# Performance work log

Measured on AMD Instinct MI355X. Metric: run time of the kernel, lower is better.

## Reference

```python
import jax, jax.numpy as jnp
import numpy as np

NEG_INF = -1e30
D_MODEL = 128


def setup_inputs() -> dict:
    key = jax.random.key(0)
    k1, k2, k3 = jax.random.split(key, 3)
    B, D, Lc, Lq = 64, D_MODEL, 1024, 256
    C = jax.random.normal(k1, (B, D, Lc), dtype=jnp.float32)
    Q = jax.random.normal(k2, (B, D, Lq), dtype=jnp.float32)
    cmask = jnp.ones((B, Lc), dtype=jnp.float32)
    qmask = jnp.ones((B, Lq), dtype=jnp.float32)
    lim = (1.0 / D) ** 0.5
    w = jax.random.uniform(k3, (3 * D,), dtype=jnp.float32, minval=-lim, maxval=lim)
    return {"C": C, "Q": Q, "cmask": cmask, "qmask": qmask, "w": w}


def reference(C, Q, cmask, qmask, w):
    # C: (B, D, Lc), Q: (B, D, Lq), w: (3D,)
    D = C.shape[1]
    Ct = jnp.swapaxes(C, 1, 2)  # (B, Lc, D)
    Qt = jnp.swapaxes(Q, 1, 2)  # (B, Lq, D)
    w1, w2, w3 = w[:D], w[D:2 * D], w[2 * D:]
    # Decomposed trilinear similarity: equivalent to cat([Ct,Qt,Ct*Qt]) @ w
    S = (jnp.einsum('bld,d->bl', Ct, w1)[:, :, None]
         + jnp.einsum('bmd,d->bm', Qt, w2)[:, None, :]
         + jnp.einsum('bld,bmd->blm', Ct * w3, Qt))  # (B, Lc, Lq)
    qm = qmask[:, None, :]  # (B, 1, Lq)
    cm = cmask[:, :, None]  # (B, Lc, 1)
    S1 = jax.nn.softmax(S + (1.0 - qm) * NEG_INF, axis=2)
    S2 = jax.nn.softmax(S + (1.0 - cm) * NEG_INF, axis=1)
    A = jnp.einsum('blm,bmd->bld', S1, Qt)  # (B, Lc, D)
    S12 = jnp.einsum('blm,bnm->bln', S1, S2)  # (B, Lc, Lc)
    Bv = jnp.einsum('bln,bnd->bld', S12, Ct)  # (B, Lc, D)
    out = jnp.concatenate([Ct, A, Ct * A, Ct * Bv], axis=2)  # (B, Lc, 4D)
    # dropout is identity in eval mode
    return jnp.swapaxes(out, 1, 2)  # (B, 4D, Lc)
```

## Files before the change

kernel.cpp:

```cpp
#include <hip/hip_runtime.h>

#define NB  64
#define ND  128
#define NLC 1024
#define NLQ 256
#define FNEG (-1e30f)

typedef __bf16 bf16x8 __attribute__((ext_vector_type(8)));
typedef float f32x4 __attribute__((ext_vector_type(4)));

__device__ __forceinline__ ushort f2bf(float x) {
  unsigned u = __float_as_uint(x);
  return (ushort)((u + 0x7fffu + ((u >> 16) & 1u)) >> 16);
}
__device__ __forceinline__ float bf2f(ushort u) {
  return __uint_as_float((unsigned)u << 16);
}
__device__ __forceinline__ bf16x8 ldfrag(const ushort* p) {
  return *reinterpret_cast<const bf16x8*>(p);
}
__device__ __forceinline__ uint4 pack8(float a0, float a1, float a2, float a3,
                                       float a4, float a5, float a6, float a7) {
  uint4 pk;
  pk.x = (unsigned)f2bf(a0) | ((unsigned)f2bf(a1) << 16);
  pk.y = (unsigned)f2bf(a2) | ((unsigned)f2bf(a3) << 16);
  pk.z = (unsigned)f2bf(a4) | ((unsigned)f2bf(a5) << 16);
  pk.w = (unsigned)f2bf(a6) | ((unsigned)f2bf(a7) << 16);
  return pk;
}

__global__ __launch_bounds__(256) void convert_kernel(
    const float* __restrict__ C, const float* __restrict__ Q,
    const float* __restrict__ w,
    ushort* __restrict__ Ctw3, ushort* __restrict__ Qt16,
    ushort* __restrict__ Cn16, ushort* __restrict__ Qn16,
    float* __restrict__ c1part, float* __restrict__ q2part) {
  __shared__ float tile[64][65];
  __shared__ float cred[64][4];
  int b = blockIdx.y;
  int tid = blockIdx.x;
  int t = threadIdx.x, c = t & 63, r0 = t >> 6;
  if (tid < 32) {
    int d0 = (tid >> 4) * 64, l0 = (tid & 15) * 64;
    const float* src = C + (size_t)b * ND * NLC;
    float part = 0.f;
#pragma unroll
    for (int p = 0; p < 16; ++p) {
      int r = r0 + p * 4;
      float v = src[(size_t)(d0 + r) * NLC + l0 + c];
      tile[c][r] = v * w[2 * ND + d0 + r];
      part += v * w[d0 + r];
    }
    cred[c][r0] = part;
    __syncthreads();
    ushort* dst = Ctw3 + (size_t)b * NLC * ND;
#pragma unroll
    for (int p = 0; p < 16; ++p) {
      int r = r0 + p * 4;
      dst[(size_t)(l0 + r) * ND + d0 + c] = f2bf(tile[r][c]);
    }
    if (t < 64)
      c1part[(size_t)(tid >> 4) * NB * NLC + b * NLC + l0 + t] =
          cred[t][0] + cred[t][1] + cred[t][2] + cred[t][3];
  } else if (tid < 40) {
    int q = tid - 32;
    int d0 = (q >> 2) * 64, m0 = (q & 3) * 64;
    const float* src = Q + (size_t)b * ND * NLQ;
    float part = 0.f;
#pragma unroll
    for (int p = 0; p < 16; ++p) {
      int r = r0 + p * 4;
      float v = src[(size_t)(d0 + r) * NLQ + m0 + c];
      tile[c][r] = v;
      part += v * w[ND + d0 + r];
    }
    cred[c][r0] = part;
    __syncthreads();
    ushort* dst = Qt16 + (size_t)b * NLQ * ND;
#pragma unroll
    for (int p = 0; p < 16; ++p) {
      int r = r0 + p * 4;
      dst[(size_t)(m0 + r) * ND + d0 + c] = f2bf(tile[r][c]);
    }
    if (t < 64)
      q2part[(size_t)(q >> 2) * NB * NLQ + b * NLQ + m0 + t] =
          cred[t][0] + cred[t][1] + cred[t][2] + cred[t][3];
  } else if (tid < 56) {
    size_t ofs = (size_t)(tid - 40) * 8192;
    const float* src = C + (size_t)b * ND * NLC + ofs;
    ushort* dst = Cn16 + (size_t)b * ND * NLC + ofs;
#pragma unroll
    for (int it = 0; it < 4; ++it) {
      int e = (it * 256 + t) * 8;
      float4 v0 = *(const float4*)(src + e), v1 = *(const float4*)(src + e + 4);
      *(uint4*)(dst + e) = pack8(v0.x, v0.y, v0.z, v0.w, v1.x, v1.y, v1.z, v1.w);
    }
  } else {
    size_t ofs = (size_t)(tid - 56) * 16384;
    const float* src = Q + (size_t)b * ND * NLQ + ofs;
    ushort* dst = Qn16 + (size_t)b * ND * NLQ + ofs;
#pragma unroll
    for (int it = 0; it < 8; ++it) {
      int e = (it * 256 + t) * 8;
      float4 v0 = *(const float4*)(src + e), v1 = *(const float4*)(src + e + 4);
      *(uint4*)(dst + e) = pack8(v0.x, v0.y, v0.z, v0.w, v1.x, v1.y, v1.z, v1.w);
    }
  }
}

__global__ __launch_bounds__(512) void score_stats(
    const ushort* __restrict__ Ctw3, const ushort* __restrict__ Qt16,
    const ushort* __restrict__ Cn16,
    const float* __restrict__ c1part, const float* __restrict__ q2part,
    const float* __restrict__ cmask, const float* __restrict__ qmask,
    ushort* __restrict__ e1g, float* __restrict__ rscale_g,
    float* __restrict__ psum_part, float* __restrict__ chunkmax_g,
    float* __restrict__ Tpart) {
  __shared__ union {
    struct { __align__(16) ushort As[128 * 32]; __align__(16) ushort Bs[256 * 32]; } s;
    __align__(16) ushort bounce[128 * 264];
    struct { __align__(16) ushort bounce2[256 * 136]; __align__(16) ushort As_c[4 * 128 * 32]; } t2;
  } u;
  __shared__ float rowred[128][4];
  __shared__ float rowsum[128][4];
  __shared__ float colred[256][2];
  __shared__ float rmaxs[128];
  __shared__ float rcs[128];
  __shared__ float cnegs[128];
  __shared__ float qnegs[256];
  __shared__ float c1s[128];
  __shared__ float q2s[256];
  __shared__ float chunkmax_s;

  int b = blockIdx.y, chunk = blockIdx.x, l0 = chunk * 128;
  int t = threadIdx.x, lane = t & 63, wid = t >> 6;
  int wy = wid >> 2, wx = wid & 3, ln = lane & 15, qd = lane >> 4;

  if (t < 128) {
    int idx = b * NLC + l0 + t;
    c1s[t] = c1part[idx] + c1part[NB * NLC + idx];
    cnegs[t] = (1.f - cmask[idx]) * FNEG;
  } else if (t < 384) {
    int m = t - 128;
    int idx = b * NLQ + m;
    q2s[m] = q2part[idx] + q2part[NB * NLQ + idx];
    qnegs[m] = (1.f - qmask[idx]) * FNEG;
  }

  const ushort* Ab = Ctw3 + (size_t)b * NLC * ND;
  const ushort* Bb = Qt16 + (size_t)b * NLQ * ND;
  f32x4 acc[4][4];
#pragma unroll
  for (int i = 0; i < 4; ++i)
#pragma unroll
    for (int j = 0; j < 4; ++j) acc[i][j] = (f32x4){0.f, 0.f, 0.f, 0.f};

  for (int kk = 0; kk < ND; kk += 32) {
#pragma unroll
    for (int p = 0; p < 3; ++p) {
      int e4 = p * 512 + t;
      if (e4 < 512) {
        int r = e4 >> 2, cc = (e4 & 3) * 8;
        *(int4*)(u.s.As + r * 32 + cc) = *(const int4*)(Ab + (size_t)(l0 + r) * ND + kk + cc);
      } else {
        int e = e4 - 512;
        int r = e >> 2, cc = (e & 3) * 8;
        *(int4*)(u.s.Bs + r * 32 + cc) = *(const int4*)(Bb + (size_t)r * ND + kk + cc);
      }
    }
    __syncthreads();
    bf16x8 af[4], bfr[4];
#pragma unroll
    for (int i = 0; i < 4; ++i) {
      af[i]  = ldfrag(u.s.As + (wy * 64 + i * 16 + ln) * 32 + qd * 8);
      bfr[i] = ldfrag(u.s.Bs + (wx * 64 + i * 16 + ln) * 32 + qd * 8);
    }
#pragma unroll
    for (int i = 0; i < 4; ++i)
#pragma unroll
      for (int j = 0; j < 4; ++j)
        acc[i][j] = __builtin_amdgcn_mfma_f32_16x16x32_bf16(af[i], bfr[j], acc[i][j], 0, 0, 0);
    __syncthreads();
  }

  float qnj[4], q2j[4];
#pragma unroll
  for (int j = 0; j < 4; ++j) {
    int m = wx * 64 + j * 16 + ln;
    qnj[j] = qnegs[m];
    q2j[j] = q2s[m];
  }
#pragma unroll
  for (int i = 0; i < 4; ++i)
#pragma unroll
    for (int r = 0; r < 4; ++r) {
      int ll = wy * 64 + i * 16 + qd * 4 + r;
      float cv = c1s[ll];
#pragma unroll
      for (int j = 0; j < 4; ++j) acc[i][j][r] += cv + q2j[j];
    }

#pragma unroll
  for (int i = 0; i < 4; ++i)
#pragma unroll
    for (int r = 0; r < 4; ++r) {
      float v = -INFINITY;
#pragma unroll
      for (int j = 0; j < 4; ++j) v = fmaxf(v, acc[i][j][r] + qnj[j]);
      v = fmaxf(v, __shfl_xor(v, 1));
      v = fmaxf(v, __shfl_xor(v, 2));
      v = fmaxf(v, __shfl_xor(v, 4));
      v = fmaxf(v, __shfl_xor(v, 8));
      if (ln == 0) rowred[wy * 64 + i * 16 + qd * 4 + r][wx] = v;
    }
  __syncthreads();
  if (t < 128) {
    float v = fmaxf(fmaxf(rowred[t][0], rowred[t][1]), fmaxf(rowred[t][2], rowred[t][3]));
    rmaxs[t] = v;
    rcs[t] = v + cnegs[t];
  }
  __syncthreads();
  if (t < 64) {
    float v = fmaxf(rcs[t], rcs[t + 64]);
    v = fmaxf(v, __shfl_xor(v, 1));
    v = fmaxf(v, __shfl_xor(v, 2));
    v = fmaxf(v, __shfl_xor(v, 4));
    v = fmaxf(v, __shfl_xor(v, 8));
    v = fmaxf(v, __shfl_xor(v, 16));
    v = fmaxf(v, __shfl_xor(v, 32));
    if (t == 0) chunkmax_s = v;
  }
  __syncthreads();
  if (t < 128) rcs[t] = __expf(rcs[t] - chunkmax_s);
  __syncthreads();

  float cs[4] = {0.f, 0.f, 0.f, 0.f};
#pragma unroll
  for (int i = 0; i < 4; ++i)
#pragma unroll
    for (int r = 0; r < 4; ++r) {
      int ll = wy * 64 + i * 16 + qd * 4 + r;
      float rmx = rmaxs[ll], rf = rcs[ll];
      float rs = 0.f;
#pragma unroll
      for (int j = 0; j < 4; ++j) {
        float e = __expf(acc[i][j][r] + qnj[j] - rmx);
        acc[i][j][r] = e;
        rs += e;
        cs[j] += e * rf;
      }
      rs += __shfl_xor(rs, 1);
      rs += __shfl_xor(rs, 2);
      rs += __shfl_xor(rs, 4);
      rs += __shfl_xor(rs, 8);
      if (ln == 0) rowsum[ll][wx] = rs;
    }
#pragma unroll
  for (int j = 0; j < 4; ++j) {
    float v = cs[j];
    v += __shfl_xor(v, 16);
    v += __shfl_xor(v, 32);
    if (qd == 0) colred[wx * 64 + j * 16 + ln][wy] = v;
  }
  __syncthreads();
  if (t < 128)
    rscale_g[b * NLC + l0 + t] =
        1.f / (rowsum[t][0] + rowsum[t][1] + rowsum[t][2] + rowsum[t][3]);
  if (t >= 256 && t < 512) {
    int m = t - 256;
    psum_part[(b * 8 + chunk) * NLQ + m] = colred[m][0] + colred[m][1];
  }
  if (t == 0) chunkmax_g[b * 8 + chunk] = chunkmax_s;

#pragma unroll
  for (int i = 0; i < 4; ++i)
#pragma unroll
    for (int r = 0; r < 4; ++r) {
      int ll = wy * 64 + i * 16 + qd * 4 + r;
#pragma unroll
      for (int j = 0; j < 4; ++j)
        u.bounce[ll * 264 + wx * 64 + j * 16 + ln] = f2bf(acc[i][j][r]);
    }
  __syncthreads();
  ushort* Eb = e1g + (size_t)b * NLC * NLQ;
#pragma unroll
  for (int p = 0; p < 8; ++p) {
    int idx4 = p * 512 + t;
    int r = idx4 >> 5, c = (idx4 & 31) * 8;
    *(int4*)(Eb + (size_t)(l0 + r) * NLQ + c) = *(const int4*)(u.bounce + r * 264 + c);
  }
  __syncthreads();

#pragma unroll
  for (int i = 0; i < 4; ++i)
#pragma unroll
    for (int r = 0; r < 4; ++r) {
      int ll = wy * 64 + i * 16 + qd * 4 + r;
      float rf = rcs[ll];
#pragma unroll
      for (int j = 0; j < 4; ++j)
        u.t2.bounce2[(wx * 64 + j * 16 + ln) * 136 + ll] = f2bf(acc[i][j][r] * rf);
    }
  {
    const ushort* Cb = Cn16 + (size_t)b * ND * NLC;
#pragma unroll
    for (int p = 0; p < 4; ++p) {
      int e4 = p * 512 + t;
      int slab = e4 >> 9, rr = (e4 >> 2) & 127, cc = (e4 & 3) * 8;
      *(int4*)(u.t2.As_c + slab * (128 * 32) + rr * 32 + cc) =
          *(const int4*)(Cb + (size_t)rr * NLC + l0 + slab * 32 + cc);
    }
  }
  __syncthreads();
  f32x4 acc2[4][4];
#pragma unroll
  for (int i = 0; i < 4; ++i)
#pragma unroll
    for (int j = 0; j < 4; ++j) acc2[i][j] = (f32x4){0.f, 0.f, 0.f, 0.f};
#pragma unroll
  for (int kk = 0; kk < 4; ++kk) {
    bf16x8 af2[4], bf2[4];
#pragma unroll
    for (int i = 0; i < 4; ++i)
      af2[i] = ldfrag(u.t2.As_c + kk * (128 * 32) + (wy * 64 + i * 16 + ln) * 32 + qd * 8);
#pragma unroll
    for (int j = 0; j < 4; ++j)
      bf2[j] = ldfrag(u.t2.bounce2 + (wx * 64 + j * 16 + ln) * 136 + kk * 32 + qd * 8);
#pragma unroll
    for (int i = 0; i < 4; ++i)
#pragma unroll
      for (int j = 0; j < 4; ++j)
        acc2[i][j] = __builtin_amdgcn_mfma_f32_16x16x32_bf16(af2[i], bf2[j], acc2[i][j], 0, 0, 0);
  }
  float* Tb = Tpart + (size_t)(b * 8 + chunk) * ND * NLQ;
#pragma unroll
  for (int i = 0; i < 4; ++i)
#pragma unroll
    for (int r = 0; r < 4; ++r) {
      int d = wy * 64 + i * 16 + qd * 4 + r;
#pragma unroll
      for (int j = 0; j < 4; ++j) {
        int m = wx * 64 + j * 16 + ln;
        Tb[(size_t)d * NLQ + m] = acc2[i][j][r];
      }
    }
}

__global__ __launch_bounds__(256) void stat_combine(
    const float* __restrict__ psum_part, const float* __restrict__ chunkmax_g,
    float* __restrict__ cinv) {
  __shared__ float cm[8];
  int b = blockIdx.x, t = threadIdx.x;
  if (t < 8) cm[t] = chunkmax_g[b * 8 + t];
  __syncthreads();
  float K = cm[0];
#pragma unroll
  for (int c = 1; c < 8; ++c) K = fmaxf(K, cm[c]);
  float s = 0.f;
#pragma unroll
  for (int c = 0; c < 8; ++c)
    s += psum_part[(b * 8 + c) * NLQ + t] * __expf(cm[c] - K);
  cinv[b * NLQ + t] = 1.f / s;
}

__global__ __launch_bounds__(256) void tcombine(
    const float* __restrict__ Tpart, const float* __restrict__ cinv,
    const float* __restrict__ chunkmax_g, ushort* __restrict__ Tt) {
  int gid = blockIdx.x * 256 + threadIdx.x;
  int e = gid * 4;
  int b = e >> 15;
  int r = e & 32767;
  int m = r & 255;
  const float* cmb = chunkmax_g + b * 8;
  float K = cmb[0];
#pragma unroll
  for (int c = 1; c < 8; ++c) K = fmaxf(K, cmb[c]);
  float4 s = {0.f, 0.f, 0.f, 0.f};
#pragma unroll
  for (int c = 0; c < 8; ++c) {
    float fac = __expf(cmb[c] - K);
    float4 v = *(const float4*)(Tpart + ((size_t)(b * 8 + c)) * ND * NLQ + r);
    s.x += fac * v.x; s.y += fac * v.y; s.z += fac * v.z; s.w += fac * v.w;
  }
  float4 ci = *(const float4*)(cinv + b * NLQ + m);
  ushort4 o;
  o.x = f2bf(s.x * ci.x); o.y = f2bf(s.y * ci.y);
  o.z = f2bf(s.z * ci.z); o.w = f2bf(s.w * ci.w);
  *(ushort4*)(Tt + (size_t)b * ND * NLQ + r) = o;
}

__global__ __launch_bounds__(512) void outk(
    const float* __restrict__ C, const ushort* __restrict__ Qn16,
    const ushort* __restrict__ Tt, const ushort* __restrict__ e1g,
    const float* __restrict__ rscale, float* __restrict__ out) {
  __shared__ __align__(16) ushort As1[128 * 32];
  __shared__ __align__(16) ushort As2[128 * 32];
  __shared__ __align__(16) ushort Bs[256 * 32];
  int b = blockIdx.y;
  int l0 = blockIdx.x * 256;
  const ushort* Qb = Qn16 + (size_t)b * ND * NLQ;
  const ushort* Tb = Tt + (size_t)b * ND * NLQ;
  const ushort* Eb = e1g + (size_t)b * NLC * NLQ;
  int t = threadIdx.x, lane = t & 63, wid = t >> 6, wy = wid >> 2, wx = wid & 3;
  int ln = lane & 15, qd = lane >> 4;
  f32x4 acc1[4][4], acc2[4][4];
#pragma unroll
  for (int i = 0; i < 4; ++i)
#pragma unroll
    for (int j = 0; j < 4; ++j) {
      acc1[i][j] = (f32x4){0.f, 0.f, 0.f, 0.f};
      acc2[i][j] = (f32x4){0.f, 0.f, 0.f, 0.f};
    }

  for (int m0 = 0; m0 < NLQ; m0 += 32) {
    {
      int r = t >> 2, cc = (t & 3) * 8;
      *(int4*)(As1 + r * 32 + cc) = *(const int4*)(Qb + (size_t)r * NLQ + m0 + cc);
      *(int4*)(As2 + r * 32 + cc) = *(const int4*)(Tb + (size_t)r * NLQ + m0 + cc);
    }
#pragma unroll
    for (int p = 0; p < 2; ++p) {
      int e4 = p * 512 + t;
      int r = e4 >> 2, cc = (e4 & 3) * 8;
      *(int4*)(Bs + r * 32 + cc) = *(const int4*)(Eb + (size_t)(l0 + r) * NLQ + m0 + cc);
    }
    __syncthreads();
    bf16x8 a1[4], a2[4], bfr[4];
#pragma unroll
    for (int i = 0; i < 4; ++i) {
      a1[i] = ldfrag(As1 + (wy * 64 + i * 16 + ln) * 32 + qd * 8);
      a2[i] = ldfrag(As2 + (wy * 64 + i * 16 + ln) * 32 + qd * 8);
      bfr[i] = ldfrag(Bs + (wx * 64 + i * 16 + ln) * 32 + qd * 8);
    }
#pragma unroll
    for (int i = 0; i < 4; ++i)
#pragma unroll
      for (int j = 0; j < 4; ++j) {
        acc1[i][j] = __builtin_amdgcn_mfma_f32_16x16x32_bf16(a1[i], bfr[j], acc1[i][j], 0, 0, 0);
        acc2[i][j] = __builtin_amdgcn_mfma_f32_16x16x32_bf16(a2[i], bfr[j], acc2[i][j], 0, 0, 0);
      }
    __syncthreads();
  }

  const float* Cb = C + (size_t)b * ND * NLC;
  float* outb = out + (size_t)b * 4 * ND * NLC;
#pragma unroll
  for (int j = 0; j < 4; ++j) {
    int l = l0 + wx * 64 + j * 16 + ln;
    float rs = rscale[b * NLC + l];
#pragma unroll
    for (int i = 0; i < 4; ++i)
#pragma unroll
      for (int r = 0; r < 4; ++r) {
        int d = wy * 64 + i * 16 + qd * 4 + r;
        float a = acc1[i][j][r] * rs;
        float bv = acc2[i][j][r] * rs;
        float c = Cb[(size_t)d * NLC + l];
        outb[(size_t)d * NLC + l] = c;
        outb[(size_t)(128 + d) * NLC + l] = a;
        outb[(size_t)(256 + d) * NLC + l] = c * a;
        outb[(size_t)(384 + d) * NLC + l] = c * bv;
      }
  }
}

extern "C" void kernel_launch(void* const* d_in, const int* in_sizes, int n_in,
                              void* d_out, int out_size, void* d_ws, size_t ws_size,
                              hipStream_t stream) {
  const float* C     = (const float*)d_in[0];
  const float* Q     = (const float*)d_in[1];
  const float* cmask = (const float*)d_in[2];
  const float* qmask = (const float*)d_in[3];
  const float* w     = (const float*)d_in[4];
  float* out = (float*)d_out;

  char* p = (char*)d_ws;
  auto alloc = [&](size_t bytes) { char* r = p; p += (bytes + 255) & ~(size_t)255; return r; };
  ushort* e1g    = (ushort*)alloc((size_t)NB * NLC * NLQ * 2);
  ushort* Ctw3   = (ushort*)alloc((size_t)NB * NLC * ND * 2);
  ushort* Qt16   = (ushort*)alloc((size_t)NB * NLQ * ND * 2);
  ushort* Cn16   = (ushort*)alloc((size_t)NB * ND * NLC * 2);
  ushort* Qn16   = (ushort*)alloc((size_t)NB * ND * NLQ * 2);
  float*  Tpart  = (float*)alloc((size_t)NB * 8 * ND * NLQ * 4);
  ushort* Tt     = (ushort*)alloc((size_t)NB * ND * NLQ * 2);
  float*  c1part = (float*)alloc((size_t)2 * NB * NLC * 4);
  float*  q2part = (float*)alloc((size_t)2 * NB * NLQ * 4);
  float*  rscale = (float*)alloc((size_t)NB * NLC * 4);
  float*  cinv   = (float*)alloc((size_t)NB * NLQ * 4);
  float*  psum   = (float*)alloc((size_t)NB * 8 * NLQ * 4);
  float*  chmax  = (float*)alloc((size_t)NB * 8 * 4);

  convert_kernel<<<dim3(58, NB), 256, 0, stream>>>(C, Q, w, Ctw3, Qt16, Cn16, Qn16,
                                                   c1part, q2part);
  score_stats<<<dim3(NLC / 128, NB), 512, 0, stream>>>(
      Ctw3, Qt16, Cn16, c1part, q2part, cmask, qmask, e1g, rscale, psum, chmax, Tpart);
  stat_combine<<<NB, 256, 0, stream>>>(psum, chmax, cinv);
  tcombine<<<(NB * ND * NLQ / 4) / 256, 256, 0, stream>>>(Tpart, cinv, chmax, Tt);
  outk<<<dim3(NLC / 256, NB), 512, 0, stream>>>(C, Qn16, Tt, e1g, rscale, out);
}
```

Before: 307.0 us.

## Register-prefetch next K tile, shrink shared memory, retile outk for occupancy

Both GEMM kernels now prefetch the next K-slice into registers while computing on the current shared-memory tile, which overlaps global loads with MFMA work. score_stats folds its reduction scratch into the shared-memory union and reads C fragments straight from global memory instead of staging them, freeing LDS so more blocks can reside per CU (launch bounds now request 4). outk is retiled to 256 threads and 128-column blocks with a min-blocks hint of 2, doubling the grid. The trade-offs are higher register pressure from the prefetch buffers, uncoalesced global fragment loads in the second GEMM, and an extra barrier.

```diff
diff --git a/kernel.cpp b/kernel.cpp
--- a/kernel.cpp
+++ b/kernel.cpp
@@ -108,7 +108,7 @@
   }
 }
 
-__global__ __launch_bounds__(512) void score_stats(
+__global__ __launch_bounds__(512, 4) void score_stats(
     const ushort* __restrict__ Ctw3, const ushort* __restrict__ Qt16,
     const ushort* __restrict__ Cn16,
     const float* __restrict__ c1part, const float* __restrict__ q2part,
@@ -118,12 +118,10 @@
     float* __restrict__ Tpart) {
   __shared__ union {
     struct { __align__(16) ushort As[128 * 32]; __align__(16) ushort Bs[256 * 32]; } s;
+    struct { float rowred[128][4]; float rowsum[128][4]; float colred[256][2]; } red;
     __align__(16) ushort bounce[128 * 264];
-    struct { __align__(16) ushort bounce2[256 * 136]; __align__(16) ushort As_c[4 * 128 * 32]; } t2;
+    __align__(16) ushort bounce2[256 * 136];
   } u;
-  __shared__ float rowred[128][4];
-  __shared__ float rowsum[128][4];
-  __shared__ float colred[256][2];
   __shared__ float rmaxs[128];
   __shared__ float rcs[128];
   __shared__ float cnegs[128];
@@ -155,20 +153,50 @@
 #pragma unroll
     for (int j = 0; j < 4; ++j) acc[i][j] = (f32x4){0.f, 0.f, 0.f, 0.f};
 
-  for (int kk = 0; kk < ND; kk += 32) {
+  int4 va[3];
+  {
 #pragma unroll
     for (int p = 0; p < 3; ++p) {
       int e4 = p * 512 + t;
       if (e4 < 512) {
         int r = e4 >> 2, cc = (e4 & 3) * 8;
-        *(int4*)(u.s.As + r * 32 + cc) = *(const int4*)(Ab + (size_t)(l0 + r) * ND + kk + cc);
+        va[p] = *(const int4*)(Ab + (size_t)(l0 + r) * ND + 0 + cc);
       } else {
         int e = e4 - 512;
         int r = e >> 2, cc = (e & 3) * 8;
-        *(int4*)(u.s.Bs + r * 32 + cc) = *(const int4*)(Bb + (size_t)r * ND + kk + cc);
-      }
-    }
+        va[p] = *(const int4*)(Bb + (size_t)r * ND + 0 + cc);
+      }
+    }
+  }
+  for (int kk = 0; kk < ND; kk += 32) {
     __syncthreads();
+#pragma unroll
+    for (int p = 0; p < 3; ++p) {
+      int e4 = p * 512 + t;
+      if (e4 < 512) {
+        int r = e4 >> 2, cc = (e4 & 3) * 8;
+        *(int4*)(u.s.As + r * 32 + cc) = va[p];
+      } else {
+        int e = e4 - 512;
+        int r = e >> 2, cc = (e & 3) * 8;
+        *(int4*)(u.s.Bs + r * 32 + cc) = va[p];
+      }
+    }
+    __syncthreads();
+    if (kk + 32 < ND) {
+#pragma unroll
+      for (int p = 0; p < 3; ++p) {
+        int e4 = p * 512 + t;
+        if (e4 < 512) {
+          int r = e4 >> 2, cc = (e4 & 3) * 8;
+          va[p] = *(const int4*)(Ab + (size_t)(l0 + r) * ND + kk + 32 + cc);
+        } else {
+          int e = e4 - 512;
+          int r = e >> 2, cc = (e & 3) * 8;
+          va[p] = *(const int4*)(Bb + (size_t)r * ND + kk + 32 + cc);
+        }
+      }
+    }
     bf16x8 af[4], bfr[4];
 #pragma unroll
     for (int i = 0; i < 4; ++i) {
@@ -180,8 +208,8 @@
 #pragma unroll
       for (int j = 0; j < 4; ++j)
         acc[i][j] = __builtin_amdgcn_mfma_f32_16x16x32_bf16(af[i], bfr[j], acc[i][j], 0, 0, 0);
-    __syncthreads();
-  }
+  }
+  __syncthreads();
 
   float qnj[4], q2j[4];
 #pragma unroll
@@ -211,11 +239,12 @@
       v = fmaxf(v, __shfl_xor(v, 2));
       v = fmaxf(v, __shfl_xor(v, 4));
       v = fmaxf(v, __shfl_xor(v, 8));
-      if (ln == 0) rowred[wy * 64 + i * 16 + qd * 4 + r][wx] = v;
+      if (ln == 0) u.red.rowred[wy * 64 + i * 16 + qd * 4 + r][wx] = v;
     }
   __syncthreads();
   if (t < 128) {
-    float v = fmaxf(fmaxf(rowred[t][0], rowred[t][1]), fmaxf(rowred[t][2], rowred[t][3]));
+    float v = fmaxf(fmaxf(u.red.rowred[t][0], u.red.rowred[t][1]),
+                    fmaxf(u.red.rowred[t][2], u.red.rowred[t][3]));
     rmaxs[t] = v;
     rcs[t] = v + cnegs[t];
   }
@@ -253,24 +282,25 @@
       rs += __shfl_xor(rs, 2);
       rs += __shfl_xor(rs, 4);
       rs += __shfl_xor(rs, 8);
-      if (ln == 0) rowsum[ll][wx] = rs;
+      if (ln == 0) u.red.rowsum[ll][wx] = rs;
     }
 #pragma unroll
   for (int j = 0; j < 4; ++j) {
     float v = cs[j];
     v += __shfl_xor(v, 16);
     v += __shfl_xor(v, 32);
-    if (qd == 0) colred[wx * 64 + j * 16 + ln][wy] = v;
+    if (qd == 0) u.red.colred[wx * 64 + j * 16 + ln][wy] = v;
   }
   __syncthreads();
   if (t < 128)
-    rscale_g[b * NLC + l0 + t] =
-        1.f / (rowsum[t][0] + rowsum[t][1] + rowsum[t][2] + rowsum[t][3]);
+    rscale_g[b * NLC + l0 + t] = 1.f / (u.red.rowsum[t][0] + u.red.rowsum[t][1] +
+                                        u.red.rowsum[t][2] + u.red.rowsum[t][3]);
   if (t >= 256 && t < 512) {
     int m = t - 256;
-    psum_part[(b * 8 + chunk) * NLQ + m] = colred[m][0] + colred[m][1];
+    psum_part[(b * 8 + chunk) * NLQ + m] = u.red.colred[m][0] + u.red.colred[m][1];
   }
   if (t == 0) chunkmax_g[b * 8 + chunk] = chunkmax_s;
+  __syncthreads();
 
 #pragma unroll
   for (int i = 0; i < 4; ++i)
@@ -299,19 +329,10 @@
       float rf = rcs[ll];
 #pragma unroll
       for (int j = 0; j < 4; ++j)
-        u.t2.bounce2[(wx * 64 + j * 16 + ln) * 136 + ll] = f2bf(acc[i][j][r] * rf);
-    }
-  {
-    const ushort* Cb = Cn16 + (size_t)b * ND * NLC;
-#pragma unroll
-    for (int p = 0; p < 4; ++p) {
-      int e4 = p * 512 + t;
-      int slab = e4 >> 9, rr = (e4 >> 2) & 127, cc = (e4 & 3) * 8;
-      *(int4*)(u.t2.As_c + slab * (128 * 32) + rr * 32 + cc) =
-          *(const int4*)(Cb + (size_t)rr * NLC + l0 + slab * 32 + cc);
-    }
-  }
-  __syncthreads();
+        u.bounce2[(wx * 64 + j * 16 + ln) * 136 + ll] = f2bf(acc[i][j][r] * rf);
+    }
+  __syncthreads();
+  const ushort* Cb = Cn16 + (size_t)b * ND * NLC;
   f32x4 acc2[4][4];
 #pragma unroll
   for (int i = 0; i < 4; ++i)
@@ -322,10 +343,10 @@
     bf16x8 af2[4], bf2[4];
 #pragma unroll
     for (int i = 0; i < 4; ++i)
-      af2[i] = ldfrag(u.t2.As_c + kk * (128 * 32) + (wy * 64 + i * 16 + ln) * 32 + qd * 8);
+      af2[i] = ldfrag(Cb + (size_t)(wy * 64 + i * 16 + ln) * NLC + l0 + kk * 32 + qd * 8);
 #pragma unroll
     for (int j = 0; j < 4; ++j)
-      bf2[j] = ldfrag(u.t2.bounce2 + (wx * 64 + j * 16 + ln) * 136 + kk * 32 + qd * 8);
+      bf2[j] = ldfrag(u.bounce2 + (wx * 64 + j * 16 + ln) * 136 + kk * 32 + qd * 8);
 #pragma unroll
     for (int i = 0; i < 4; ++i)
 #pragma unroll
@@ -389,19 +410,19 @@
   *(ushort4*)(Tt + (size_t)b * ND * NLQ + r) = o;
 }
 
-__global__ __launch_bounds__(512) void outk(
+__global__ __launch_bounds__(256, 2) void outk(
     const float* __restrict__ C, const ushort* __restrict__ Qn16,
     const ushort* __restrict__ Tt, const ushort* __restrict__ e1g,
     const float* __restrict__ rscale, float* __restrict__ out) {
   __shared__ __align__(16) ushort As1[128 * 32];
   __shared__ __align__(16) ushort As2[128 * 32];
-  __shared__ __align__(16) ushort Bs[256 * 32];
+  __shared__ __align__(16) ushort Bs[128 * 32];
   int b = blockIdx.y;
-  int l0 = blockIdx.x * 256;
+  int l0 = blockIdx.x * 128;
   const ushort* Qb = Qn16 + (size_t)b * ND * NLQ;
   const ushort* Tb = Tt + (size_t)b * ND * NLQ;
   const ushort* Eb = e1g + (size_t)b * NLC * NLQ;
-  int t = threadIdx.x, lane = t & 63, wid = t >> 6, wy = wid >> 2, wx = wid & 3;
+  int t = threadIdx.x, lane = t & 63, wid = t >> 6, wy = wid >> 1, wx = wid & 1;
   int ln = lane & 15, qd = lane >> 4;
   f32x4 acc1[4][4], acc2[4][4];
 #pragma unroll
@@ -412,19 +433,35 @@
       acc2[i][j] = (f32x4){0.f, 0.f, 0.f, 0.f};
     }
 
+  int4 v1[2], v2[2], v3[2];
+#pragma unroll
+  for (int p = 0; p < 2; ++p) {
+    int e = t * 8 + p * 2048;
+    int r = e >> 5, cc = e & 31;
+    v1[p] = *(const int4*)(Qb + (size_t)r * NLQ + cc);
+    v2[p] = *(const int4*)(Tb + (size_t)r * NLQ + cc);
+    v3[p] = *(const int4*)(Eb + (size_t)(l0 + r) * NLQ + cc);
+  }
   for (int m0 = 0; m0 < NLQ; m0 += 32) {
-    {
-      int r = t >> 2, cc = (t & 3) * 8;
-      *(int4*)(As1 + r * 32 + cc) = *(const int4*)(Qb + (size_t)r * NLQ + m0 + cc);
-      *(int4*)(As2 + r * 32 + cc) = *(const int4*)(Tb + (size_t)r * NLQ + m0 + cc);
-    }
+    __syncthreads();
 #pragma unroll
     for (int p = 0; p < 2; ++p) {
-      int e4 = p * 512 + t;
-      int r = e4 >> 2, cc = (e4 & 3) * 8;
-      *(int4*)(Bs + r * 32 + cc) = *(const int4*)(Eb + (size_t)(l0 + r) * NLQ + m0 + cc);
+      int e = t * 8 + p * 2048;
+      *(int4*)(As1 + e) = v1[p];
+      *(int4*)(As2 + e) = v2[p];
+      *(int4*)(Bs + e)  = v3[p];
     }
     __syncthreads();
+    if (m0 + 32 < NLQ) {
+#pragma unroll
+      for (int p = 0; p < 2; ++p) {
+        int e = t * 8 + p * 2048;
+        int r = e >> 5, cc = e & 31;
+        v1[p] = *(const int4*)(Qb + (size_t)r * NLQ + m0 + 32 + cc);
+        v2[p] = *(const int4*)(Tb + (size_t)r * NLQ + m0 + 32 + cc);
+        v3[p] = *(const int4*)(Eb + (size_t)(l0 + r) * NLQ + m0 + 32 + cc);
+      }
+    }
     bf16x8 a1[4], a2[4], bfr[4];
 #pragma unroll
     for (int i = 0; i < 4; ++i) {
@@ -439,7 +476,6 @@
         acc1[i][j] = __builtin_amdgcn_mfma_f32_16x16x32_bf16(a1[i], bfr[j], acc1[i][j], 0, 0, 0);
         acc2[i][j] = __builtin_amdgcn_mfma_f32_16x16x32_bf16(a2[i], bfr[j], acc2[i][j], 0, 0, 0);
       }
-    __syncthreads();
   }
 
   const float* Cb = C + (size_t)b * ND * NLC;
@@ -496,5 +532,5 @@
       Ctw3, Qt16, Cn16, c1part, q2part, cmask, qmask, e1g, rscale, psum, chmax, Tpart);
   stat_combine<<<NB, 256, 0, stream>>>(psum, chmax, cinv);
   tcombine<<<(NB * ND * NLQ / 4) / 256, 256, 0, stream>>>(Tpart, cinv, chmax, Tt);
-  outk<<<dim3(NLC / 256, NB), 512, 0, stream>>>(C, Qn16, Tt, e1g, rscale, out);
-}
+  outk<<<dim3(NLC / 128, NB), 256, 0, stream>>>(C, Qn16, Tt, e1g, rscale, out);
+}
```

Result: slower. 337.2 us (+9.8%).

## Coalesce output epilogue via LDS, move C copy to convert, shrink LDS

Applied to the files above, without the earlier changes.

The output kernel now stages the scaled A and Bv tiles through shared memory and writes the three derived output slabs with coalesced float4 stores, instead of scattered per-element stores. The plain C slice of the output is written in the convert kernel, which already reads C, so the output kernel no longer copies it. The output kernel tile is halved to 128 columns to double its block count. score_stats unions its reduction buffers with the staging buffers and loads the C operand fragments straight from global memory rather than staging them in LDS, lowering LDS use. Both kernels get a min-blocks launch bound hint, which may force register spilling.

```diff
diff --git a/kernel.cpp b/kernel.cpp
--- a/kernel.cpp
+++ b/kernel.cpp
@@ -34,7 +34,8 @@
     const float* __restrict__ w,
     ushort* __restrict__ Ctw3, ushort* __restrict__ Qt16,
     ushort* __restrict__ Cn16, ushort* __restrict__ Qn16,
-    float* __restrict__ c1part, float* __restrict__ q2part) {
+    float* __restrict__ c1part, float* __restrict__ q2part,
+    float* __restrict__ out) {
   __shared__ float tile[64][65];
   __shared__ float cred[64][4];
   int b = blockIdx.y;
@@ -43,6 +44,7 @@
   if (tid < 32) {
     int d0 = (tid >> 4) * 64, l0 = (tid & 15) * 64;
     const float* src = C + (size_t)b * ND * NLC;
+    float* o0 = out + (size_t)b * 4 * ND * NLC;
     float part = 0.f;
 #pragma unroll
     for (int p = 0; p < 16; ++p) {
@@ -50,6 +52,7 @@
       float v = src[(size_t)(d0 + r) * NLC + l0 + c];
       tile[c][r] = v * w[2 * ND + d0 + r];
       part += v * w[d0 + r];
+      o0[(size_t)(d0 + r) * NLC + l0 + c] = v;
     }
     cred[c][r0] = part;
     __syncthreads();
@@ -108,7 +111,7 @@
   }
 }
 
-__global__ __launch_bounds__(512) void score_stats(
+__global__ __launch_bounds__(512, 4) void score_stats(
     const ushort* __restrict__ Ctw3, const ushort* __restrict__ Qt16,
     const ushort* __restrict__ Cn16,
     const float* __restrict__ c1part, const float* __restrict__ q2part,
@@ -118,12 +121,10 @@
     float* __restrict__ Tpart) {
   __shared__ union {
     struct { __align__(16) ushort As[128 * 32]; __align__(16) ushort Bs[256 * 32]; } s;
+    struct { float rowred[128][4]; float rowsum[128][4]; float colred[256][2]; } red;
     __align__(16) ushort bounce[128 * 264];
-    struct { __align__(16) ushort bounce2[256 * 136]; __align__(16) ushort As_c[4 * 128 * 32]; } t2;
+    __align__(16) ushort bounce2[256 * 136];
   } u;
-  __shared__ float rowred[128][4];
-  __shared__ float rowsum[128][4];
-  __shared__ float colred[256][2];
   __shared__ float rmaxs[128];
   __shared__ float rcs[128];
   __shared__ float cnegs[128];
@@ -211,11 +212,12 @@
       v = fmaxf(v, __shfl_xor(v, 2));
       v = fmaxf(v, __shfl_xor(v, 4));
       v = fmaxf(v, __shfl_xor(v, 8));
-      if (ln == 0) rowred[wy * 64 + i * 16 + qd * 4 + r][wx] = v;
+      if (ln == 0) u.red.rowred[wy * 64 + i * 16 + qd * 4 + r][wx] = v;
     }
   __syncthreads();
   if (t < 128) {
-    float v = fmaxf(fmaxf(rowred[t][0], rowred[t][1]), fmaxf(rowred[t][2], rowred[t][3]));
+    float v = fmaxf(fmaxf(u.red.rowred[t][0], u.red.rowred[t][1]),
+                    fmaxf(u.red.rowred[t][2], u.red.rowred[t][3]));
     rmaxs[t] = v;
     rcs[t] = v + cnegs[t];
   }
@@ -253,24 +255,25 @@
       rs += __shfl_xor(rs, 2);
       rs += __shfl_xor(rs, 4);
       rs += __shfl_xor(rs, 8);
-      if (ln == 0) rowsum[ll][wx] = rs;
+      if (ln == 0) u.red.rowsum[ll][wx] = rs;
     }
 #pragma unroll
   for (int j = 0; j < 4; ++j) {
     float v = cs[j];
     v += __shfl_xor(v, 16);
     v += __shfl_xor(v, 32);
-    if (qd == 0) colred[wx * 64 + j * 16 + ln][wy] = v;
+    if (qd == 0) u.red.colred[wx * 64 + j * 16 + ln][wy] = v;
   }
   __syncthreads();
   if (t < 128)
-    rscale_g[b * NLC + l0 + t] =
-        1.f / (rowsum[t][0] + rowsum[t][1] + rowsum[t][2] + rowsum[t][3]);
+    rscale_g[b * NLC + l0 + t] = 1.f / (u.red.rowsum[t][0] + u.red.rowsum[t][1] +
+                                        u.red.rowsum[t][2] + u.red.rowsum[t][3]);
   if (t >= 256 && t < 512) {
     int m = t - 256;
-    psum_part[(b * 8 + chunk) * NLQ + m] = colred[m][0] + colred[m][1];
+    psum_part[(b * 8 + chunk) * NLQ + m] = u.red.colred[m][0] + u.red.colred[m][1];
   }
   if (t == 0) chunkmax_g[b * 8 + chunk] = chunkmax_s;
+  __syncthreads();
 
 #pragma unroll
   for (int i = 0; i < 4; ++i)
@@ -299,19 +302,10 @@
       float rf = rcs[ll];
 #pragma unroll
       for (int j = 0; j < 4; ++j)
-        u.t2.bounce2[(wx * 64 + j * 16 + ln) * 136 + ll] = f2bf(acc[i][j][r] * rf);
-    }
-  {
-    const ushort* Cb = Cn16 + (size_t)b * ND * NLC;
-#pragma unroll
-    for (int p = 0; p < 4; ++p) {
-      int e4 = p * 512 + t;
-      int slab = e4 >> 9, rr = (e4 >> 2) & 127, cc = (e4 & 3) * 8;
-      *(int4*)(u.t2.As_c + slab * (128 * 32) + rr * 32 + cc) =
-          *(const int4*)(Cb + (size_t)rr * NLC + l0 + slab * 32 + cc);
-    }
-  }
-  __syncthreads();
+        u.bounce2[(wx * 64 + j * 16 + ln) * 136 + ll] = f2bf(acc[i][j][r] * rf);
+    }
+  __syncthreads();
+  const ushort* Cb = Cn16 + (size_t)b * ND * NLC;
   f32x4 acc2[4][4];
 #pragma unroll
   for (int i = 0; i < 4; ++i)
@@ -322,10 +316,10 @@
     bf16x8 af2[4], bf2[4];
 #pragma unroll
     for (int i = 0; i < 4; ++i)
-      af2[i] = ldfrag(u.t2.As_c + kk * (128 * 32) + (wy * 64 + i * 16 + ln) * 32 + qd * 8);
+      af2[i] = ldfrag(Cb + (size_t)(wy * 64 + i * 16 + ln) * NLC + l0 + kk * 32 + qd * 8);
 #pragma unroll
     for (int j = 0; j < 4; ++j)
-      bf2[j] = ldfrag(u.t2.bounce2 + (wx * 64 + j * 16 + ln) * 136 + kk * 32 + qd * 8);
+      bf2[j] = ldfrag(u.bounce2 + (wx * 64 + j * 16 + ln) * 136 + kk * 32 + qd * 8);
 #pragma unroll
     for (int i = 0; i < 4; ++i)
 #pragma unroll
@@ -389,25 +383,28 @@
   *(ushort4*)(Tt + (size_t)b * ND * NLQ + r) = o;
 }
 
-__global__ __launch_bounds__(512) void outk(
+__global__ __launch_bounds__(512, 4) void outk(
     const float* __restrict__ C, const ushort* __restrict__ Qn16,
     const ushort* __restrict__ Tt, const ushort* __restrict__ e1g,
     const float* __restrict__ rscale, float* __restrict__ out) {
-  __shared__ __align__(16) ushort As1[128 * 32];
-  __shared__ __align__(16) ushort As2[128 * 32];
-  __shared__ __align__(16) ushort Bs[256 * 32];
+  __shared__ union {
+    struct { __align__(16) ushort As1[128 * 32]; __align__(16) ushort As2[128 * 32];
+             __align__(16) ushort Bs[128 * 32]; } st;
+    struct { float a[32][132]; float bv[32][132]; } ep;
+  } u;
   int b = blockIdx.y;
-  int l0 = blockIdx.x * 256;
+  int l0 = blockIdx.x * 128;
   const ushort* Qb = Qn16 + (size_t)b * ND * NLQ;
   const ushort* Tb = Tt + (size_t)b * ND * NLQ;
   const ushort* Eb = e1g + (size_t)b * NLC * NLQ;
-  int t = threadIdx.x, lane = t & 63, wid = t >> 6, wy = wid >> 2, wx = wid & 3;
+  int t = threadIdx.x, lane = t & 63, wid = t >> 6;
+  int wy = wid >> 2, wx = wid & 3;
   int ln = lane & 15, qd = lane >> 4;
-  f32x4 acc1[4][4], acc2[4][4];
-#pragma unroll
-  for (int i = 0; i < 4; ++i)
-#pragma unroll
-    for (int j = 0; j < 4; ++j) {
+  f32x4 acc1[4][2], acc2[4][2];
+#pragma unroll
+  for (int i = 0; i < 4; ++i)
+#pragma unroll
+    for (int j = 0; j < 2; ++j) {
       acc1[i][j] = (f32x4){0.f, 0.f, 0.f, 0.f};
       acc2[i][j] = (f32x4){0.f, 0.f, 0.f, 0.f};
     }
@@ -415,52 +412,75 @@
   for (int m0 = 0; m0 < NLQ; m0 += 32) {
     {
       int r = t >> 2, cc = (t & 3) * 8;
-      *(int4*)(As1 + r * 32 + cc) = *(const int4*)(Qb + (size_t)r * NLQ + m0 + cc);
-      *(int4*)(As2 + r * 32 + cc) = *(const int4*)(Tb + (size_t)r * NLQ + m0 + cc);
-    }
-#pragma unroll
-    for (int p = 0; p < 2; ++p) {
-      int e4 = p * 512 + t;
-      int r = e4 >> 2, cc = (e4 & 3) * 8;
-      *(int4*)(Bs + r * 32 + cc) = *(const int4*)(Eb + (size_t)(l0 + r) * NLQ + m0 + cc);
-    }
-    __syncthreads();
-    bf16x8 a1[4], a2[4], bfr[4];
+      *(int4*)(u.st.As1 + r * 32 + cc) = *(const int4*)(Qb + (size_t)r * NLQ + m0 + cc);
+      *(int4*)(u.st.As2 + r * 32 + cc) = *(const int4*)(Tb + (size_t)r * NLQ + m0 + cc);
+      *(int4*)(u.st.Bs + r * 32 + cc)  = *(const int4*)(Eb + (size_t)(l0 + r) * NLQ + m0 + cc);
+    }
+    __syncthreads();
+    bf16x8 a1[4], a2[4], bfr[2];
 #pragma unroll
     for (int i = 0; i < 4; ++i) {
-      a1[i] = ldfrag(As1 + (wy * 64 + i * 16 + ln) * 32 + qd * 8);
-      a2[i] = ldfrag(As2 + (wy * 64 + i * 16 + ln) * 32 + qd * 8);
-      bfr[i] = ldfrag(Bs + (wx * 64 + i * 16 + ln) * 32 + qd * 8);
-    }
+      a1[i] = ldfrag(u.st.As1 + (wy * 64 + i * 16 + ln) * 32 + qd * 8);
+      a2[i] = ldfrag(u.st.As2 + (wy * 64 + i * 16 + ln) * 32 + qd * 8);
+    }
+#pragma unroll
+    for (int j = 0; j < 2; ++j)
+      bfr[j] = ldfrag(u.st.Bs + (wx * 32 + j * 16 + ln) * 32 + qd * 8);
 #pragma unroll
     for (int i = 0; i < 4; ++i)
 #pragma unroll
-      for (int j = 0; j < 4; ++j) {
+      for (int j = 0; j < 2; ++j) {
         acc1[i][j] = __builtin_amdgcn_mfma_f32_16x16x32_bf16(a1[i], bfr[j], acc1[i][j], 0, 0, 0);
         acc2[i][j] = __builtin_amdgcn_mfma_f32_16x16x32_bf16(a2[i], bfr[j], acc2[i][j], 0, 0, 0);
       }
     __syncthreads();
   }
 
-  const float* Cb = C + (size_t)b * ND * NLC;
+  float rsj[2];
+#pragma unroll
+  for (int j = 0; j < 2; ++j)
+    rsj[j] = rscale[b * NLC + l0 + wx * 32 + j * 16 + ln];
+
+  const float* Cbase = C + (size_t)b * ND * NLC;
   float* outb = out + (size_t)b * 4 * ND * NLC;
 #pragma unroll
-  for (int j = 0; j < 4; ++j) {
-    int l = l0 + wx * 64 + j * 16 + ln;
-    float rs = rscale[b * NLC + l];
-#pragma unroll
-    for (int i = 0; i < 4; ++i)
-#pragma unroll
-      for (int r = 0; r < 4; ++r) {
-        int d = wy * 64 + i * 16 + qd * 4 + r;
-        float a = acc1[i][j][r] * rs;
-        float bv = acc2[i][j][r] * rs;
-        float c = Cb[(size_t)d * NLC + l];
-        outb[(size_t)d * NLC + l] = c;
-        outb[(size_t)(128 + d) * NLC + l] = a;
-        outb[(size_t)(256 + d) * NLC + l] = c * a;
-        outb[(size_t)(384 + d) * NLC + l] = c * bv;
+  for (int db = 0; db < 4; ++db) {
+    __syncthreads();
+    if (wy == (db >> 1)) {
+      int ibase = (db & 1) * 2;
+#pragma unroll
+      for (int ii = 0; ii < 2; ++ii) {
+        int i = ibase + ii;
+#pragma unroll
+        for (int j = 0; j < 2; ++j) {
+          int lc = wx * 32 + j * 16 + ln;
+#pragma unroll
+          for (int r = 0; r < 4; ++r) {
+            int dr = ii * 16 + qd * 4 + r;
+            u.ep.a[dr][lc]  = acc1[i][j][r] * rsj[j];
+            u.ep.bv[dr][lc] = acc2[i][j][r] * rsj[j];
+          }
+        }
       }
+    }
+    __syncthreads();
+    int row = t >> 4, colf = (t & 15) * 8;
+    int d = db * 32 + row;
+    const float* Crow = Cbase + (size_t)d * NLC + l0 + colf;
+    float4 c0 = *(const float4*)(Crow), c1 = *(const float4*)(Crow + 4);
+    float4 a0 = *(const float4*)&u.ep.a[row][colf];
+    float4 a1v = *(const float4*)&u.ep.a[row][colf + 4];
+    float4 b0 = *(const float4*)&u.ep.bv[row][colf];
+    float4 b1 = *(const float4*)&u.ep.bv[row][colf + 4];
+    float* oA = outb + (size_t)(128 + d) * NLC + l0 + colf;
+    float* oCA = outb + (size_t)(256 + d) * NLC + l0 + colf;
+    float* oCB = outb + (size_t)(384 + d) * NLC + l0 + colf;
+    *(float4*)(oA) = a0;
+    *(float4*)(oA + 4) = a1v;
+    *(float4*)(oCA) = (float4){c0.x * a0.x, c0.y * a0.y, c0.z * a0.z, c0.w * a0.w};
+    *(float4*)(oCA + 4) = (float4){c1.x * a1v.x, c1.y * a1v.y, c1.z * a1v.z, c1.w * a1v.w};
+    *(float4*)(oCB) = (float4){c0.x * b0.x, c0.y * b0.y, c0.z * b0.z, c0.w * b0.w};
+    *(float4*)(oCB + 4) = (float4){c1.x * b1.x, c1.y * b1.y, c1.z * b1.z, c1.w * b1.w};
   }
 }
 
@@ -491,10 +511,10 @@
   float*  chmax  = (float*)alloc((size_t)NB * 8 * 4);
 
   convert_kernel<<<dim3(58, NB), 256, 0, stream>>>(C, Q, w, Ctw3, Qt16, Cn16, Qn16,
-                                                   c1part, q2part);
+                                                   c1part, q2part, out);
   score_stats<<<dim3(NLC / 128, NB), 512, 0, stream>>>(
       Ctw3, Qt16, Cn16, c1part, q2part, cmask, qmask, e1g, rscale, psum, chmax, Tpart);
   stat_combine<<<NB, 256, 0, stream>>>(psum, chmax, cinv);
   tcombine<<<(NB * ND * NLQ / 4) / 256, 256, 0, stream>>>(Tpart, cinv, chmax, Tt);
-  outk<<<dim3(NLC / 256, NB), 512, 0, stream>>>(C, Qn16, Tt, e1g, rscale, out);
-}
+  outk<<<dim3(NLC / 128, NB), 512, 0, stream>>>(C, Qn16, Tt, e1g, rscale, out);
+}
```

Measured after the change: 267.1 us. 13.0% less time.
